# Optimization experiments

Measured on AMD Instinct MI355X. Metric: run time of the kernel, lower is better.

The kernel has to match this reference:

```python
import jax, jax.numpy as jnp
import numpy as np

B, T, F = 64, 512, 256
ENC = 256      # encoder output dim
P = 128        # projection_dim
H = 256        # gru_hidden_dim
K = 12         # num_future_steps
TEMP = 0.1


def setup_inputs() -> dict:
    key = jax.random.key(0)
    ks = jax.random.split(key, 12)
    s = lambda *d: 1.0 / np.sqrt(d[0])
    return {
        "x_seq": jax.random.normal(ks[0], (B, T, F), jnp.float32),
        # encoder: Dense(F -> ENC)
        "W_enc": jax.random.normal(ks[1], (F, ENC), jnp.float32) * s(F),
        "b_enc": jnp.zeros((ENC,), jnp.float32),
        # projection: Dense(ENC -> P)
        "W_proj": jax.random.normal(ks[2], (ENC, P), jnp.float32) * s(ENC),
        "b_proj": jnp.zeros((P,), jnp.float32),
        # GRUCell (flax convention: input dense has bias, hidden dense bias only on n)
        "Wi": jax.random.normal(ks[3], (P, 3 * H), jnp.float32) * s(P),
        "bi": jnp.zeros((3 * H,), jnp.float32),
        "Wh": jax.random.normal(ks[4], (H, 3 * H), jnp.float32) * s(H),
        "bhn": jnp.zeros((H,), jnp.float32),
        # K predictors: Dense(H -> P)
        "Wp": jax.random.normal(ks[5], (K, H, P), jnp.float32) * s(H),
        "bp": jnp.zeros((K, P), jnp.float32),
    }


def _gru_scan(z_seq, Wi, bi, Wh, bhn):
    # z_seq: [B, T, P] -> c_seq: [B, T, H]
    def step(h, x_t):
        gi = x_t @ Wi + bi          # [B, 3H]
        gh = h @ Wh                 # [B, 3H]
        ir, iz, inn = jnp.split(gi, 3, axis=-1)
        hr, hz, hn = jnp.split(gh, 3, axis=-1)
        r = jax.nn.sigmoid(ir + hr)
        z = jax.nn.sigmoid(iz + hz)
        n = jnp.tanh(inn + r * (hn + bhn))
        h_new = (1.0 - z) * n + z * h
        return h_new, h_new

    h0 = jnp.zeros((z_seq.shape[0], Wh.shape[0]), z_seq.dtype)
    _, c = jax.lax.scan(step, h0, jnp.swapaxes(z_seq, 0, 1))  # c: [T, B, H]
    return jnp.swapaxes(c, 0, 1)


def reference(x_seq, W_enc, b_enc, W_proj, b_proj, Wi, bi, Wh, bhn, Wp, bp):
    # encoder per timestep (vmap(vmap(Dense)) == batched matmul)
    z_seq = x_seq @ W_enc + b_enc                 # [B, T, ENC]
    z_seq = z_seq @ W_proj + b_proj               # [B, T, P]
    c_seq = _gru_scan(z_seq, Wi, bi, Wh, bhn)     # [B, T, H]

    Tlen = z_seq.shape[1]
    loss = jnp.asarray(0.0, z_seq.dtype)
    for k in range(1, K + 1):
        if Tlen - k <= 0:
            continue
        z_pos = z_seq[:, k:]                      # [B, T-k, P]
        pred = c_seq[:, :-k] @ Wp[k - 1] + bp[k - 1]  # [B, T-k, P]
        logits = jnp.einsum('btd,bkd->btk', pred, z_pos) / TEMP
        labels = jnp.arange(logits.shape[1])
        # NOTE: faithful to source: [..., labels] with labels=arange is an
        # identity gather along the last axis (not a diagonal pick).
        loss = loss + jnp.mean(-jax.nn.log_softmax(logits, axis=-1)[..., labels])
    return loss / K
```

## Files before the change

### kernel.cpp

```cpp
#include <hip/hip_runtime.h>
#include <hip/hip_bf16.h>
#include <math.h>

#define B_   64
#define T_   512
#define F_   256
#define ENC_ 256
#define P_   128
#define H_   256
#define K_   12
#define INV_TEMP 10.0f

typedef unsigned short u16;
typedef _Float16 half2v __attribute__((ext_vector_type(2)));
union U2H { unsigned int u; half2v h; };
typedef __attribute__((ext_vector_type(8))) short bf16x8;
typedef __attribute__((ext_vector_type(4))) float f32x4;
typedef _Float16 f16x8 __attribute__((ext_vector_type(8)));
union BF8 { bf16x8 v; u16 e[8]; };

__device__ __forceinline__ float rcpf(float x) {
#if __has_builtin(__builtin_amdgcn_rcpf)
    return __builtin_amdgcn_rcpf(x);
#else
    return 1.f / x;
#endif
}
__device__ __forceinline__ u16 f2bf(float f) {
    unsigned int u = __float_as_uint(f);
    unsigned int r = (u + 0x7fffu + ((u >> 16) & 1u)) >> 16;
    return (u16)r;
}
__device__ __forceinline__ float bf2f(u16 v) {
    return __uint_as_float(((unsigned int)v) << 16);
}
__device__ __forceinline__ float bflo(unsigned int u) { return __uint_as_float(u << 16); }
__device__ __forceinline__ float bfhi(unsigned int u) { return __uint_as_float(u & 0xffff0000u); }
__device__ __forceinline__ float wave_sum(float v) {
    #pragma unroll
    for (int o = 32; o > 0; o >>= 1) v += __shfl_down(v, o, 64);
    return v;
}

__global__ __launch_bounds__(256) void setup_conv(const float* __restrict__ Wh,
                                                  _Float16* __restrict__ Wht,
                                                  const float* __restrict__ Wi,
                                                  u16* __restrict__ Wit,
                                                  const float* __restrict__ Wp,
                                                  u16* __restrict__ Wpt,
                                                  const float* __restrict__ We,
                                                  const float* __restrict__ be,
                                                  const float* __restrict__ Wpj,
                                                  const float* __restrict__ bpj,
                                                  u16* __restrict__ Wct,
                                                  float* __restrict__ bc,
                                                  float* __restrict__ accum) {
    int bid = blockIdx.x;
    if (bid < 192) {
        __shared__ float tile0[32][33];
        int g0 = (bid % 24) * 32, k0 = (bid / 24) * 32;
        int tx = threadIdx.x & 31, ty = threadIdx.x >> 5;
        #pragma unroll
        for (int i = 0; i < 32; i += 8)
            tile0[ty + i][tx] = Wh[(size_t)(k0 + ty + i) * 768 + g0 + tx];
        __syncthreads();
        #pragma unroll
        for (int i = 0; i < 32; i += 8)
            Wht[(size_t)(g0 + ty + i) * 256 + k0 + tx] = (_Float16)tile0[tx][ty + i];
    } else if (bid < 288) {
        __shared__ float tile[32][33];
        int b2 = bid - 192;
        int n0 = (b2 % 24) * 32, k0 = (b2 / 24) * 32;
        int tx = threadIdx.x & 31, ty = threadIdx.x >> 5;
        #pragma unroll
        for (int i = 0; i < 32; i += 8)
            tile[ty + i][tx] = Wi[(size_t)(k0 + ty + i) * 768 + n0 + tx];
        __syncthreads();
        #pragma unroll
        for (int i = 0; i < 32; i += 8)
            Wit[(size_t)(n0 + ty + i) * 128 + k0 + tx] = f2bf(tile[tx][ty + i]);
    } else if (bid < 672) {
        __shared__ float tile2[32][33];
        int b3 = bid - 288;
        int kq = b3 / 32, rem = b3 % 32;
        int h0 = (rem % 8) * 32, p0 = (rem / 8) * 32;
        int tx = threadIdx.x & 31, ty = threadIdx.x >> 5;
        #pragma unroll
        for (int i = 0; i < 32; i += 8)
            tile2[ty + i][tx] = Wp[(size_t)kq * H_ * P_ + (size_t)(h0 + ty + i) * P_ + p0 + tx];
        __syncthreads();
        #pragma unroll
        for (int i = 0; i < 32; i += 8)
            Wpt[(size_t)kq * P_ * H_ + (size_t)(p0 + ty + i) * H_ + h0 + tx] = f2bf(tile2[tx][ty + i]);
    } else {
        int f = (bid - 672) * 2 + (threadIdx.x >> 7);
        int p = threadIdx.x & 127;
        if (f < F_) {
            float a = 0.f;
            for (int e = 0; e < ENC_; e++) a = fmaf(We[f * ENC_ + e], Wpj[e * P_ + p], a);
            Wct[(size_t)p * F_ + f] = f2bf(a);
        } else if (f == F_) {
            float a = bpj[p];
            for (int e = 0; e < ENC_; e++) a = fmaf(be[e], Wpj[e * P_ + p], a);
            bc[p] = a;
        } else {
            #pragma unroll
            for (int i = 0; i < 8; i++) accum[p * 8 + i] = 0.f;
        }
    }
}

__global__ __launch_bounds__(256) void gemm_mfma_f32a(const float* __restrict__ A,
                                                      const u16* __restrict__ Bt,
                                                      const float* __restrict__ bias,
                                                      u16* __restrict__ Ch,
                                                      int N, int K) {
    int tid  = threadIdx.x;
    int w    = tid >> 6;
    int lane = tid & 63;
    int col  = lane & 15;
    int quad = lane >> 4;
    int bm = blockIdx.y * 64, bn = blockIdx.x * 128;

    f32x4 acc[8] = {};
    const float* arow = A + (size_t)(bm + w * 16 + col) * K;
    #pragma unroll
    for (int k0 = 0; k0 < K; k0 += 32) {
        float4 v0 = *(const float4*)(arow + k0 + quad * 8);
        float4 v1 = *(const float4*)(arow + k0 + quad * 8 + 4);
        BF8 af;
        af.e[0] = f2bf(v0.x); af.e[1] = f2bf(v0.y); af.e[2] = f2bf(v0.z); af.e[3] = f2bf(v0.w);
        af.e[4] = f2bf(v1.x); af.e[5] = f2bf(v1.y); af.e[6] = f2bf(v1.z); af.e[7] = f2bf(v1.w);
        #pragma unroll
        for (int nt = 0; nt < 8; nt++) {
            bf16x8 bf = *(const bf16x8*)(Bt + (size_t)(bn + nt * 16 + col) * K + k0 + quad * 8);
            acc[nt] = __builtin_amdgcn_mfma_f32_16x16x32_bf16(af.v, bf, acc[nt], 0, 0, 0);
        }
    }
    #pragma unroll
    for (int nt = 0; nt < 8; nt++) {
        int gn = bn + nt * 16 + col;
        float bv = bias[gn];
        #pragma unroll
        for (int r = 0; r < 4; r++) {
            int gm = bm + w * 16 + quad * 4 + r;
            Ch[(size_t)gm * N + gn] = f2bf(acc[nt][r] + bv);
        }
    }
}

__global__ __launch_bounds__(256) void gemm_mfma(const u16* __restrict__ A,
                                                 const u16* __restrict__ Bt,
                                                 const float* __restrict__ bias,
                                                 u16* __restrict__ Ch,
                                                 int N, int K) {
    int tid  = threadIdx.x;
    int w    = tid >> 6;
    int lane = tid & 63;
    int col  = lane & 15;
    int quad = lane >> 4;
    int bm = blockIdx.y * 64, bn = blockIdx.x * 128;

    f32x4 acc[8] = {};
    const u16* arow = A + (size_t)(bm + w * 16 + col) * K;
    #pragma unroll
    for (int k0 = 0; k0 < K; k0 += 32) {
        bf16x8 af = *(const bf16x8*)(arow + k0 + quad * 8);
        #pragma unroll
        for (int nt = 0; nt < 8; nt++) {
            bf16x8 bf = *(const bf16x8*)(Bt + (size_t)(bn + nt * 16 + col) * K + k0 + quad * 8);
            acc[nt] = __builtin_amdgcn_mfma_f32_16x16x32_bf16(af, bf, acc[nt], 0, 0, 0);
        }
    }
    #pragma unroll
    for (int nt = 0; nt < 8; nt++) {
        int gn = bn + nt * 16 + col;
        float bv = bias[gn];
        #pragma unroll
        for (int r = 0; r < 4; r++) {
            int gm = bm + w * 16 + quad * 4 + r;
            Ch[(size_t)gm * N + gn] = f2bf(acc[nt][r] + bv);
        }
    }
}

#define GRUB_ 64

__global__ __attribute__((amdgpu_flat_work_group_size(512, 512)))
void gru_zsum_kernel(const u16* __restrict__ gi,
                     const _Float16* __restrict__ Wht,
                     const float* __restrict__ bhn,
                     u16* __restrict__ ch,
                     const u16* __restrict__ zh,
                     float* __restrict__ zsum) {
    __shared__ __align__(16) char smem[8704];
    int tid = threadIdx.x;

    if (blockIdx.x >= GRUB_) {
        float (*part)[128] = (float (*)[128])smem;
        int b   = blockIdx.x - GRUB_;
        int pg  = tid & 31;
        int g   = tid >> 5;
        const u16* zb = zh + (size_t)b * T_ * P_;
        float s0 = 0.f, s1 = 0.f, s2 = 0.f, s3 = 0.f;
        for (int t = 1 + g; t < T_; t += 16) {
            uint2 v = *(const uint2*)(zb + (size_t)t * P_ + pg * 4);
            s0 += bflo(v.x); s1 += bfhi(v.x);
            s2 += bflo(v.y); s3 += bfhi(v.y);
        }
        part[g][pg * 4 + 0] = s0; part[g][pg * 4 + 1] = s1;
        part[g][pg * 4 + 2] = s2; part[g][pg * 4 + 3] = s3;
        __syncthreads();
        if (tid < 128) {
            float s = 0.f;
            #pragma unroll
            for (int g2 = 0; g2 < 16; g2++) s += part[g2][tid];
            zsum[(size_t)b * P_ + tid] = s;
        }
        return;
    }

    _Float16* hbase = (_Float16*)smem;

    int lane = tid & 63, w = tid >> 6;
    int col  = lane & 15, quad = lane >> 4;
    int b    = blockIdx.x;
    int jj0  = w * 32 + col;

    f16x8 wf[3][2][8];
    #pragma unroll
    for (int g = 0; g < 3; g++)
        #pragma unroll
        for (int n2 = 0; n2 < 2; n2++) {
            const _Float16* src = Wht + (size_t)(g * 256 + jj0 + n2 * 16) * 256 + quad * 8;
            #pragma unroll
            for (int k0 = 0; k0 < 8; k0++)
                wf[g][n2][k0] = *(const f16x8*)(src + k0 * 32);
        }
    #pragma unroll
    for (int g = 0; g < 3; g++)
        #pragma unroll
        for (int n2 = 0; n2 < 2; n2++)
            #pragma unroll
            for (int k0 = 0; k0 < 8; k0++)
                asm volatile("" : "+v"(wf[g][n2][k0]));

    for (int i = tid; i < 528; i += 512) hbase[i] = (_Float16)0.f;

    const u16* gb = gi + (size_t)b * T_ * 768;
    u16* cb       = ch + (size_t)b * T_ * 256;
    float bh0 = bhn[jj0], bh1 = bhn[jj0 + 16];
    float hold0 = 0.f, hold1 = 0.f;
    unsigned int pf[2][6];

    {
        pf[0][0] = gb[jj0];        pf[0][1] = gb[jj0 + 16];
        pf[0][2] = gb[256 + jj0];  pf[0][3] = gb[256 + jj0 + 16];
        pf[0][4] = gb[512 + jj0];  pf[0][5] = gb[512 + jj0 + 16];
    }
    __syncthreads();

    auto body = [&](int t, int c, int pt) {
        int n = c ^ 1;
        if (pt < T_) {
            const u16* gr = gb + (size_t)pt * 768;
            pf[n][0] = gr[jj0];        pf[n][1] = gr[jj0 + 16];
            pf[n][2] = gr[256 + jj0];  pf[n][3] = gr[256 + jj0 + 16];
            pf[n][4] = gr[512 + jj0];  pf[n][5] = gr[512 + jj0 + 16];
        }
        const _Float16* HC = hbase + c * 264;
        _Float16*       HN = hbase + n * 264;
        f32x4 aR0 = {}, aR1 = {}, aZ0 = {}, aZ1 = {}, aN0 = {}, aN1 = {};
        #pragma unroll
        for (int k0 = 0; k0 < 8; k0++) {
            f16x8 af = *(const f16x8*)(HC + k0 * 32 + quad * 8);
            aR0 = __builtin_amdgcn_mfma_f32_16x16x32_f16(af, wf[0][0][k0], aR0, 0, 0, 0);
            aR1 = __builtin_amdgcn_mfma_f32_16x16x32_f16(af, wf[0][1][k0], aR1, 0, 0, 0);
            aZ0 = __builtin_amdgcn_mfma_f32_16x16x32_f16(af, wf[1][0][k0], aZ0, 0, 0, 0);
            aZ1 = __builtin_amdgcn_mfma_f32_16x16x32_f16(af, wf[1][1][k0], aZ1, 0, 0, 0);
            aN0 = __builtin_amdgcn_mfma_f32_16x16x32_f16(af, wf[2][0][k0], aN0, 0, 0, 0);
            aN1 = __builtin_amdgcn_mfma_f32_16x16x32_f16(af, wf[2][1][k0], aN1, 0, 0, 0);
        }
        float rg0 = rcpf(1.f + __expf(-(bf2f((u16)pf[c][0]) + aR0[0])));
        float rg1 = rcpf(1.f + __expf(-(bf2f((u16)pf[c][1]) + aR1[0])));
        float zg0 = rcpf(1.f + __expf(-(bf2f((u16)pf[c][2]) + aZ0[0])));
        float zg1 = rcpf(1.f + __expf(-(bf2f((u16)pf[c][3]) + aZ1[0])));
        float xn0 = bf2f((u16)pf[c][4]) + rg0 * (aN0[0] + bh0);
        float xn1 = bf2f((u16)pf[c][5]) + rg1 * (aN1[0] + bh1);
        float nn0 = fmaf(2.f, rcpf(1.f + __expf(-2.f * xn0)), -1.f);
        float nn1 = fmaf(2.f, rcpf(1.f + __expf(-2.f * xn1)), -1.f);
        hold0 = (1.f - zg0) * nn0 + zg0 * hold0;
        hold1 = (1.f - zg1) * nn1 + zg1 * hold1;
        if (quad == 0) {
            HN[jj0]      = (_Float16)hold0;
            HN[jj0 + 16] = (_Float16)hold1;
        } else if (quad == 1) {
            u16* cr = cb + (size_t)t * 256;
            cr[jj0]      = f2bf(hold0);
            cr[jj0 + 16] = f2bf(hold1);
        }
        asm volatile("s_waitcnt lgkmcnt(0)" ::: "memory");
        __builtin_amdgcn_s_barrier();
        asm volatile("" ::: "memory");
    };

    #pragma unroll 1
    for (int t = 0; t < T_; t += 2) {
        body(t,     0, t + 1);
        body(t + 1, 1, t + 2);
    }
}

__global__ __launch_bounds__(512) void loss_fused(const u16* __restrict__ ch,
                                                  const u16* __restrict__ Wpt,
                                                  const float* __restrict__ bp,
                                                  const u16* __restrict__ zh,
                                                  const float* __restrict__ zsum,
                                                  float* __restrict__ accum) {
    __shared__ u16 Pst[128][136];
    __shared__ u16 Zt[64][136];
    __shared__ float sS[128];
    __shared__ float red[8];
    int k  = blockIdx.z + 1;
    int b  = blockIdx.y;
    int t0 = blockIdx.x * 128;
    int Tk = T_ - k;
    int tid  = threadIdx.x;
    int w    = tid >> 6;
    int lane = tid & 63;
    int col  = lane & 15;
    int quad = lane >> 4;
    const u16* zb = zh + (size_t)b * T_ * P_;

    if (tid < 128) {
        float s = zsum[(size_t)b * P_ + tid];
        for (int t = 1; t < k; t++) s -= bf2f(zb[(size_t)t * P_ + tid]);
        sS[tid] = s;
    }

    {
        f32x4 acc[8] = {};
        const u16* arow = ch + ((size_t)b * T_ + t0 + w * 16 + col) * H_;
        const u16* wk   = Wpt + (size_t)(k - 1) * P_ * H_;
        #pragma unroll
        for (int k0 = 0; k0 < 8; k0++) {
            bf16x8 af = *(const bf16x8*)(arow + k0 * 32 + quad * 8);
            #pragma unroll
            for (int nt = 0; nt < 8; nt++) {
                bf16x8 bf = *(const bf16x8*)(wk + (size_t)(nt * 16 + col) * H_ + k0 * 32 + quad * 8);
                acc[nt] = __builtin_amdgcn_mfma_f32_16x16x32_bf16(af, bf, acc[nt], 0, 0, 0);
            }
        }
        #pragma unroll
        for (int nt = 0; nt < 8; nt++) {
            float bias = bp[(size_t)(k - 1) * P_ + nt * 16 + col];
            #pragma unroll
            for (int r = 0; r < 4; r++)
                Pst[w * 16 + quad * 4 + r][nt * 16 + col] = f2bf(acc[nt][r] + bias);
        }
    }
    __syncthreads();

    float mloc[4], sloc[4];
    #pragma unroll
    for (int r = 0; r < 4; r++) { mloc[r] = -INFINITY; sloc[r] = 0.f; }

    for (int ct = 0; ct < Tk; ct += 64) {
        __syncthreads();
        {
            int cc = tid;
            #pragma unroll
            for (int rep = 0; rep < 2; rep++, cc += 512) {
                int row = cc >> 4;
                int off = (cc & 15) * 8;
                int tcol = k + ct + row;
                *(uint4*)&Zt[row][off] = *(const uint4*)(zb + (size_t)tcol * P_ + off);
            }
        }
        __syncthreads();
        f32x4 acc[4] = {};
        #pragma unroll
        for (int k0 = 0; k0 < 4; k0++) {
            bf16x8 af = *(const bf16x8*)(&Pst[w * 16 + col][k0 * 32 + quad * 8]);
            #pragma unroll
            for (int nt = 0; nt < 4; nt++) {
                bf16x8 bf = *(const bf16x8*)(&Zt[nt * 16 + col][k0 * 32 + quad * 8]);
                acc[nt] = __builtin_amdgcn_mfma_f32_16x16x32_bf16(af, bf, acc[nt], 0, 0, 0);
            }
        }
        #pragma unroll
        for (int r = 0; r < 4; r++) {
            float l[4];
            float tmax = -INFINITY;
            #pragma unroll
            for (int nt = 0; nt < 4; nt++) {
                bool valid = (ct + nt * 16 + col) < Tk;
                l[nt] = valid ? acc[nt][r] * INV_TEMP : -INFINITY;
                tmax = fmaxf(tmax, l[nt]);
            }
            float mnew = fmaxf(mloc[r], tmax);
            float e = __expf(l[0] - mnew) + __expf(l[1] - mnew)
                    + __expf(l[2] - mnew) + __expf(l[3] - mnew);
            sloc[r] = sloc[r] * __expf(mloc[r] - mnew) + e;
            mloc[r] = mnew;
        }
    }
    #pragma unroll
    for (int r = 0; r < 4; r++) {
        #pragma unroll
        for (int o = 1; o < 16; o <<= 1) {
            float mo = __shfl_xor(mloc[r], o, 64);
            float so = __shfl_xor(sloc[r], o, 64);
            float mn = fmaxf(mloc[r], mo);
            sloc[r] = sloc[r] * __expf(mloc[r] - mn) + so * __expf(mo - mn);
            mloc[r] = mn;
        }
    }
    float tkinv = INV_TEMP / (float)Tk;
    float scale = 1.0f / ((float)K_ * (float)B_ * (float)Tk);
    float bs = 0.f;
    #pragma unroll
    for (int r = 0; r < 4; r++) {
        int row = w * 16 + quad * 4 + r;
        BF8 pv;
        pv.v = *(const bf16x8*)(&Pst[row][col * 8]);
        float d = 0.f;
        #pragma unroll
        for (int m = 0; m < 8; m++) d = fmaf(bf2f(pv.e[m]), sS[col * 8 + m], d);
        #pragma unroll
        for (int o = 1; o < 16; o <<= 1) d += __shfl_xor(d, o, 64);
        int gr = t0 + row;
        if (gr < Tk) bs += mloc[r] + __logf(sloc[r]) - d * tkinv;
    }
    if (col != 0) bs = 0.f;
    bs = wave_sum(bs);
    if (lane == 0) red[w] = bs;
    __syncthreads();
    if (tid == 0) {
        float tot = 0.f;
        #pragma unroll
        for (int i = 0; i < 8; i++) tot += red[i];
        atomicAdd(&accum[(blockIdx.x * 809 + b * 67 + blockIdx.z * 131) & 1023],
                  tot * scale);
    }
}

__global__ void finalize(const float* __restrict__ accum, float* __restrict__ out) {
    int tid = threadIdx.x;
    __shared__ float red[4];
    float v = 0.f;
    for (int i = tid; i < 1024; i += 256) v += accum[i];
    float sres = wave_sum(v);
    if ((tid & 63) == 0) red[tid >> 6] = sres;
    __syncthreads();
    if (tid == 0) out[0] = red[0] + red[1] + red[2] + red[3];
}

extern "C" void kernel_launch(void* const* d_in, const int* in_sizes, int n_in,
                              void* d_out, int out_size, void* d_ws, size_t ws_size,
                              hipStream_t stream) {
    const float* x      = (const float*)d_in[0];
    const float* W_enc  = (const float*)d_in[1];
    const float* b_enc  = (const float*)d_in[2];
    const float* W_proj = (const float*)d_in[3];
    const float* b_proj = (const float*)d_in[4];
    const float* Wi     = (const float*)d_in[5];
    const float* bi     = (const float*)d_in[6];
    const float* Wh     = (const float*)d_in[7];
    const float* bhn    = (const float*)d_in[8];
    const float* Wp     = (const float*)d_in[9];
    const float* bp     = (const float*)d_in[10];
    float* out = (float*)d_out;

    float* ws    = (float*)d_ws;
    float* bc    = ws;
    float* accum = bc + 128;
    _Float16* Wht = (_Float16*)(ws + 1152);
    u16* Wct     = (u16*)(ws + 99456);
    u16* Wit     = (u16*)(ws + 115840);
    u16* Wpt     = (u16*)(ws + 164992);
    u16* zh      = (u16*)(ws + 361600);
    float* zsum  = ws + 2458752;
    u16* gi      = (u16*)(ws + 2466944);
    u16* ch      = (u16*)(ws + 15049856);

    const int MT = B_ * T_;

    setup_conv<<<801, 256, 0, stream>>>(Wh, Wht, Wi, Wit, Wp, Wpt,
                                        W_enc, b_enc, W_proj, b_proj, Wct, bc, accum);
    gemm_mfma_f32a<<<dim3(1, MT / 64), 256, 0, stream>>>(x, Wct, bc, zh, P_, F_);
    gemm_mfma<<<dim3(6, MT / 64), 256, 0, stream>>>(zh, Wit, bi, gi, 3 * H_, P_);
    gru_zsum_kernel<<<GRUB_ + B_, 512, 0, stream>>>(gi, Wht, bhn, ch, zh, zsum);
    loss_fused<<<dim3(4, B_, K_), 512, 0, stream>>>(ch, Wpt, bp, zh, zsum, accum);
    finalize<<<1, 256, 0, stream>>>(accum, out);
}
```

Baseline: 953.6 us.

## Process three future steps per loss block sharing Z tiles; move GRU gate prefetch

The loss kernel now handles three prediction offsets per block, so each staged Z tile is reused by three MFMA chains. The grid shrinks from 12 to 4 in z, and the next Z tile is held in registers while the current one is computed. In the GRU kernel, the next step's gate inputs are now loaded at the end of each step rather than double-buffered at the start, which shortens the per-step register footprint. The trade-offs are triple the shared memory and accumulator registers in the loss kernel, which may lower occupancy, and GRU global loads that now sit closer to the barrier.

New measurement: 1.040 ms. 1.09x slower.

```diff
diff --git a/kernel.cpp b/kernel.cpp
--- a/kernel.cpp
+++ b/kernel.cpp
@@ -251,23 +251,17 @@
     u16* cb       = ch + (size_t)b * T_ * 256;
     float bh0 = bhn[jj0], bh1 = bhn[jj0 + 16];
     float hold0 = 0.f, hold1 = 0.f;
-    unsigned int pf[2][6];
+    unsigned int pf[6];
 
     {
-        pf[0][0] = gb[jj0];        pf[0][1] = gb[jj0 + 16];
-        pf[0][2] = gb[256 + jj0];  pf[0][3] = gb[256 + jj0 + 16];
-        pf[0][4] = gb[512 + jj0];  pf[0][5] = gb[512 + jj0 + 16];
+        pf[0] = gb[jj0];        pf[1] = gb[jj0 + 16];
+        pf[2] = gb[256 + jj0];  pf[3] = gb[256 + jj0 + 16];
+        pf[4] = gb[512 + jj0];  pf[5] = gb[512 + jj0 + 16];
     }
     __syncthreads();
 
-    auto body = [&](int t, int c, int pt) {
+    auto body = [&](int t, int c) {
         int n = c ^ 1;
-        if (pt < T_) {
-            const u16* gr = gb + (size_t)pt * 768;
-            pf[n][0] = gr[jj0];        pf[n][1] = gr[jj0 + 16];
-            pf[n][2] = gr[256 + jj0];  pf[n][3] = gr[256 + jj0 + 16];
-            pf[n][4] = gr[512 + jj0];  pf[n][5] = gr[512 + jj0 + 16];
-        }
         const _Float16* HC = hbase + c * 264;
         _Float16*       HN = hbase + n * 264;
         f32x4 aR0 = {}, aR1 = {}, aZ0 = {}, aZ1 = {}, aN0 = {}, aN1 = {};
@@ -281,12 +275,12 @@
             aN0 = __builtin_amdgcn_mfma_f32_16x16x32_f16(af, wf[2][0][k0], aN0, 0, 0, 0);
             aN1 = __builtin_amdgcn_mfma_f32_16x16x32_f16(af, wf[2][1][k0], aN1, 0, 0, 0);
         }
-        float rg0 = rcpf(1.f + __expf(-(bf2f((u16)pf[c][0]) + aR0[0])));
-        float rg1 = rcpf(1.f + __expf(-(bf2f((u16)pf[c][1]) + aR1[0])));
-        float zg0 = rcpf(1.f + __expf(-(bf2f((u16)pf[c][2]) + aZ0[0])));
-        float zg1 = rcpf(1.f + __expf(-(bf2f((u16)pf[c][3]) + aZ1[0])));
-        float xn0 = bf2f((u16)pf[c][4]) + rg0 * (aN0[0] + bh0);
-        float xn1 = bf2f((u16)pf[c][5]) + rg1 * (aN1[0] + bh1);
+        float rg0 = rcpf(1.f + __expf(-(bf2f((u16)pf[0]) + aR0[0])));
+        float rg1 = rcpf(1.f + __expf(-(bf2f((u16)pf[1]) + aR1[0])));
+        float zg0 = rcpf(1.f + __expf(-(bf2f((u16)pf[2]) + aZ0[0])));
+        float zg1 = rcpf(1.f + __expf(-(bf2f((u16)pf[3]) + aZ1[0])));
+        float xn0 = bf2f((u16)pf[4]) + rg0 * (aN0[0] + bh0);
+        float xn1 = bf2f((u16)pf[5]) + rg1 * (aN1[0] + bh1);
         float nn0 = fmaf(2.f, rcpf(1.f + __expf(-2.f * xn0)), -1.f);
         float nn1 = fmaf(2.f, rcpf(1.f + __expf(-2.f * xn1)), -1.f);
         hold0 = (1.f - zg0) * nn0 + zg0 * hold0;
@@ -299,6 +293,12 @@
             cr[jj0]      = f2bf(hold0);
             cr[jj0 + 16] = f2bf(hold1);
         }
+        if (t + 1 < T_) {
+            const u16* gr = gb + (size_t)(t + 1) * 768;
+            pf[0] = gr[jj0];        pf[1] = gr[jj0 + 16];
+            pf[2] = gr[256 + jj0];  pf[3] = gr[256 + jj0 + 16];
+            pf[4] = gr[512 + jj0];  pf[5] = gr[512 + jj0 + 16];
+        }
         asm volatile("s_waitcnt lgkmcnt(0)" ::: "memory");
         __builtin_amdgcn_s_barrier();
         asm volatile("" ::: "memory");
@@ -306,25 +306,26 @@
 
     #pragma unroll 1
     for (int t = 0; t < T_; t += 2) {
-        body(t,     0, t + 1);
-        body(t + 1, 1, t + 2);
-    }
-}
-
-__global__ __launch_bounds__(512) void loss_fused(const u16* __restrict__ ch,
-                                                  const u16* __restrict__ Wpt,
-                                                  const float* __restrict__ bp,
-                                                  const u16* __restrict__ zh,
-                                                  const float* __restrict__ zsum,
-                                                  float* __restrict__ accum) {
-    __shared__ u16 Pst[128][136];
+        body(t,     0);
+        body(t + 1, 1);
+    }
+}
+
+__global__ __attribute__((amdgpu_flat_work_group_size(512, 512)))
+void loss_fused(const u16* __restrict__ ch,
+                const u16* __restrict__ Wpt,
+                const float* __restrict__ bp,
+                const u16* __restrict__ zh,
+                const float* __restrict__ zsum,
+                float* __restrict__ accum) {
+    __shared__ u16 Pst[3][128][136];
     __shared__ u16 Zt[64][136];
-    __shared__ float sS[128];
+    __shared__ float sS[3][128];
     __shared__ float red[8];
-    int k  = blockIdx.z + 1;
+    int kz    = blockIdx.z;
+    int kbase = 1 + kz * 3;
     int b  = blockIdx.y;
     int t0 = blockIdx.x * 128;
-    int Tk = T_ - k;
     int tid  = threadIdx.x;
     int w    = tid >> 6;
     int lane = tid & 63;
@@ -332,105 +333,132 @@
     int quad = lane >> 4;
     const u16* zb = zh + (size_t)b * T_ * P_;
 
+    int row0 = tid >> 4;
+    int row1 = row0 + 32;
+    int off  = (tid & 15) * 8;
+    uint4 rA = *(const uint4*)(zb + (size_t)(kbase + row0) * P_ + off);
+    uint4 rB = *(const uint4*)(zb + (size_t)(kbase + row1) * P_ + off);
+
     if (tid < 128) {
         float s = zsum[(size_t)b * P_ + tid];
-        for (int t = 1; t < k; t++) s -= bf2f(zb[(size_t)t * P_ + tid]);
-        sS[tid] = s;
+        for (int t = 1; t < kbase; t++) s -= bf2f(zb[(size_t)t * P_ + tid]);
+        sS[0][tid] = s;
+        s -= bf2f(zb[(size_t)kbase * P_ + tid]);       sS[1][tid] = s;
+        s -= bf2f(zb[(size_t)(kbase + 1) * P_ + tid]); sS[2][tid] = s;
     }
 
     {
-        f32x4 acc[8] = {};
+        f32x4 acc[3][8] = {};
         const u16* arow = ch + ((size_t)b * T_ + t0 + w * 16 + col) * H_;
-        const u16* wk   = Wpt + (size_t)(k - 1) * P_ * H_;
+        const u16* wk   = Wpt + (size_t)(kbase - 1) * P_ * H_;
         #pragma unroll
         for (int k0 = 0; k0 < 8; k0++) {
             bf16x8 af = *(const bf16x8*)(arow + k0 * 32 + quad * 8);
             #pragma unroll
+            for (int j = 0; j < 3; j++)
+                #pragma unroll
+                for (int nt = 0; nt < 8; nt++) {
+                    bf16x8 bf = *(const bf16x8*)(wk + (size_t)j * P_ * H_
+                                 + (size_t)(nt * 16 + col) * H_ + k0 * 32 + quad * 8);
+                    acc[j][nt] = __builtin_amdgcn_mfma_f32_16x16x32_bf16(af, bf, acc[j][nt], 0, 0, 0);
+                }
+        }
+        #pragma unroll
+        for (int j = 0; j < 3; j++)
+            #pragma unroll
             for (int nt = 0; nt < 8; nt++) {
-                bf16x8 bf = *(const bf16x8*)(wk + (size_t)(nt * 16 + col) * H_ + k0 * 32 + quad * 8);
-                acc[nt] = __builtin_amdgcn_mfma_f32_16x16x32_bf16(af, bf, acc[nt], 0, 0, 0);
+                float bias = bp[(size_t)(kbase - 1 + j) * P_ + nt * 16 + col];
+                #pragma unroll
+                for (int r = 0; r < 4; r++)
+                    Pst[j][w * 16 + quad * 4 + r][nt * 16 + col] = f2bf(acc[j][nt][r] + bias);
             }
-        }
-        #pragma unroll
-        for (int nt = 0; nt < 8; nt++) {
-            float bias = bp[(size_t)(k - 1) * P_ + nt * 16 + col];
-            #pragma unroll
-            for (int r = 0; r < 4; r++)
-                Pst[w * 16 + quad * 4 + r][nt * 16 + col] = f2bf(acc[nt][r] + bias);
-        }
     }
     __syncthreads();
 
-    float mloc[4], sloc[4];
-    #pragma unroll
-    for (int r = 0; r < 4; r++) { mloc[r] = -INFINITY; sloc[r] = 0.f; }
-
-    for (int ct = 0; ct < Tk; ct += 64) {
+    float mloc[3][4], sloc[3][4];
+    #pragma unroll
+    for (int j = 0; j < 3; j++)
+        #pragma unroll
+        for (int r = 0; r < 4; r++) { mloc[j][r] = -INFINITY; sloc[j][r] = 0.f; }
+
+    int TkMax = T_ - kbase;
+    for (int ct = 0; ct < TkMax; ct += 64) {
         __syncthreads();
-        {
-            int cc = tid;
-            #pragma unroll
-            for (int rep = 0; rep < 2; rep++, cc += 512) {
-                int row = cc >> 4;
-                int off = (cc & 15) * 8;
-                int tcol = k + ct + row;
-                *(uint4*)&Zt[row][off] = *(const uint4*)(zb + (size_t)tcol * P_ + off);
-            }
-        }
+        *(uint4*)&Zt[row0][off] = rA;
+        *(uint4*)&Zt[row1][off] = rB;
         __syncthreads();
-        f32x4 acc[4] = {};
+        if (ct + 64 < TkMax) {
+            int tc = kbase + ct + 64;
+            rA = *(const uint4*)(zb + (size_t)(tc + row0) * P_ + off);
+            rB = *(const uint4*)(zb + (size_t)(tc + row1) * P_ + off);
+        }
+        f32x4 acc[3][4] = {};
         #pragma unroll
         for (int k0 = 0; k0 < 4; k0++) {
-            bf16x8 af = *(const bf16x8*)(&Pst[w * 16 + col][k0 * 32 + quad * 8]);
+            bf16x8 pa0 = *(const bf16x8*)(&Pst[0][w * 16 + col][k0 * 32 + quad * 8]);
+            bf16x8 pa1 = *(const bf16x8*)(&Pst[1][w * 16 + col][k0 * 32 + quad * 8]);
+            bf16x8 pa2 = *(const bf16x8*)(&Pst[2][w * 16 + col][k0 * 32 + quad * 8]);
             #pragma unroll
             for (int nt = 0; nt < 4; nt++) {
                 bf16x8 bf = *(const bf16x8*)(&Zt[nt * 16 + col][k0 * 32 + quad * 8]);
-                acc[nt] = __builtin_amdgcn_mfma_f32_16x16x32_bf16(af, bf, acc[nt], 0, 0, 0);
+                acc[0][nt] = __builtin_amdgcn_mfma_f32_16x16x32_bf16(pa0, bf, acc[0][nt], 0, 0, 0);
+                acc[1][nt] = __builtin_amdgcn_mfma_f32_16x16x32_bf16(pa1, bf, acc[1][nt], 0, 0, 0);
+                acc[2][nt] = __builtin_amdgcn_mfma_f32_16x16x32_bf16(pa2, bf, acc[2][nt], 0, 0, 0);
             }
         }
         #pragma unroll
+        for (int j = 0; j < 3; j++) {
+            #pragma unroll
+            for (int r = 0; r < 4; r++) {
+                float l[4];
+                float tmax = -INFINITY;
+                #pragma unroll
+                for (int nt = 0; nt < 4; nt++) {
+                    int cc = ct + nt * 16 + col;
+                    bool v = (cc >= j) && (kbase + cc < T_);
+                    l[nt] = v ? acc[j][nt][r] * INV_TEMP : -INFINITY;
+                    tmax = fmaxf(tmax, l[nt]);
+                }
+                float mnew = fmaxf(mloc[j][r], tmax);
+                float e = __expf(l[0] - mnew) + __expf(l[1] - mnew)
+                        + __expf(l[2] - mnew) + __expf(l[3] - mnew);
+                sloc[j][r] = sloc[j][r] * __expf(mloc[j][r] - mnew) + e;
+                mloc[j][r] = mnew;
+            }
+        }
+    }
+    #pragma unroll
+    for (int j = 0; j < 3; j++)
+        #pragma unroll
         for (int r = 0; r < 4; r++) {
-            float l[4];
-            float tmax = -INFINITY;
-            #pragma unroll
-            for (int nt = 0; nt < 4; nt++) {
-                bool valid = (ct + nt * 16 + col) < Tk;
-                l[nt] = valid ? acc[nt][r] * INV_TEMP : -INFINITY;
-                tmax = fmaxf(tmax, l[nt]);
+            #pragma unroll
+            for (int o = 1; o < 16; o <<= 1) {
+                float mo = __shfl_xor(mloc[j][r], o, 64);
+                float so = __shfl_xor(sloc[j][r], o, 64);
+                float mn = fmaxf(mloc[j][r], mo);
+                sloc[j][r] = sloc[j][r] * __expf(mloc[j][r] - mn) + so * __expf(mo - mn);
+                mloc[j][r] = mn;
             }
-            float mnew = fmaxf(mloc[r], tmax);
-            float e = __expf(l[0] - mnew) + __expf(l[1] - mnew)
-                    + __expf(l[2] - mnew) + __expf(l[3] - mnew);
-            sloc[r] = sloc[r] * __expf(mloc[r] - mnew) + e;
-            mloc[r] = mnew;
-        }
-    }
-    #pragma unroll
-    for (int r = 0; r < 4; r++) {
-        #pragma unroll
-        for (int o = 1; o < 16; o <<= 1) {
-            float mo = __shfl_xor(mloc[r], o, 64);
-            float so = __shfl_xor(sloc[r], o, 64);
-            float mn = fmaxf(mloc[r], mo);
-            sloc[r] = sloc[r] * __expf(mloc[r] - mn) + so * __expf(mo - mn);
-            mloc[r] = mn;
-        }
-    }
-    float tkinv = INV_TEMP / (float)Tk;
-    float scale = 1.0f / ((float)K_ * (float)B_ * (float)Tk);
+        }
     float bs = 0.f;
     #pragma unroll
-    for (int r = 0; r < 4; r++) {
-        int row = w * 16 + quad * 4 + r;
-        BF8 pv;
-        pv.v = *(const bf16x8*)(&Pst[row][col * 8]);
-        float d = 0.f;
-        #pragma unroll
-        for (int m = 0; m < 8; m++) d = fmaf(bf2f(pv.e[m]), sS[col * 8 + m], d);
-        #pragma unroll
-        for (int o = 1; o < 16; o <<= 1) d += __shfl_xor(d, o, 64);
-        int gr = t0 + row;
-        if (gr < Tk) bs += mloc[r] + __logf(sloc[r]) - d * tkinv;
+    for (int j = 0; j < 3; j++) {
+        int Tkj = T_ - (kbase + j);
+        float tkinv = INV_TEMP / (float)Tkj;
+        float scale = 1.0f / ((float)K_ * (float)B_ * (float)Tkj);
+        #pragma unroll
+        for (int r = 0; r < 4; r++) {
+            int row = w * 16 + quad * 4 + r;
+            BF8 pv;
+            pv.v = *(const bf16x8*)(&Pst[j][row][col * 8]);
+            float d = 0.f;
+            #pragma unroll
+            for (int m = 0; m < 8; m++) d = fmaf(bf2f(pv.e[m]), sS[j][col * 8 + m], d);
+            #pragma unroll
+            for (int o = 1; o < 16; o <<= 1) d += __shfl_xor(d, o, 64);
+            int gr = t0 + row;
+            if (gr < Tkj) bs += (mloc[j][r] + __logf(sloc[j][r]) - d * tkinv) * scale;
+        }
     }
     if (col != 0) bs = 0.f;
     bs = wave_sum(bs);
@@ -440,8 +468,7 @@
         float tot = 0.f;
         #pragma unroll
         for (int i = 0; i < 8; i++) tot += red[i];
-        atomicAdd(&accum[(blockIdx.x * 809 + b * 67 + blockIdx.z * 131) & 1023],
-                  tot * scale);
+        atomicAdd(&accum[(blockIdx.x * 809 + b * 67 + blockIdx.z * 131) & 1023], tot);
     }
 }
 
@@ -491,6 +518,6 @@
     gemm_mfma_f32a<<<dim3(1, MT / 64), 256, 0, stream>>>(x, Wct, bc, zh, P_, F_);
     gemm_mfma<<<dim3(6, MT / 64), 256, 0, stream>>>(zh, Wit, bi, gi, 3 * H_, P_);
     gru_zsum_kernel<<<GRUB_ + B_, 512, 0, stream>>>(gi, Wht, bhn, ch, zh, zsum);
-    loss_fused<<<dim3(4, B_, K_), 512, 0, stream>>>(ch, Wpt, bp, zh, zsum, accum);
+    loss_fused<<<dim3(4, B_, 4), 512, 0, stream>>>(ch, Wpt, bp, zh, zsum, accum);
     finalize<<<1, 256, 0, stream>>>(accum, out);
 }
```

## Double-buffer Z tiles in loss kernel and move GRU gate prefetch after compute

Applied to the files above, without the earlier changes.

The loss kernel now keeps two shared-memory Z tiles, prefetching the next chunks into registers two iterations ahead and swapping buffers with a single barrier per iteration instead of two. It also sets a minimum-occupancy hint in launch bounds. In the GRU scan, the double-buffered register prefetch of input gates is replaced by a single set loaded after the gate math, just before the step barrier, which lowers register use but leaves less time to hide that load. The extra register prefetch and the occupancy hint may cause spilling in the loss kernel.

Measured after the change: 967.8 us. No clear change (+1.5%).

```diff
diff --git a/kernel.cpp b/kernel.cpp
--- a/kernel.cpp
+++ b/kernel.cpp
@@ -251,23 +251,17 @@
     u16* cb       = ch + (size_t)b * T_ * 256;
     float bh0 = bhn[jj0], bh1 = bhn[jj0 + 16];
     float hold0 = 0.f, hold1 = 0.f;
-    unsigned int pf[2][6];
+    unsigned int pf[6];
 
     {
-        pf[0][0] = gb[jj0];        pf[0][1] = gb[jj0 + 16];
-        pf[0][2] = gb[256 + jj0];  pf[0][3] = gb[256 + jj0 + 16];
-        pf[0][4] = gb[512 + jj0];  pf[0][5] = gb[512 + jj0 + 16];
+        pf[0] = gb[jj0];        pf[1] = gb[jj0 + 16];
+        pf[2] = gb[256 + jj0];  pf[3] = gb[256 + jj0 + 16];
+        pf[4] = gb[512 + jj0];  pf[5] = gb[512 + jj0 + 16];
     }
     __syncthreads();
 
-    auto body = [&](int t, int c, int pt) {
+    auto body = [&](int t, int c) {
         int n = c ^ 1;
-        if (pt < T_) {
-            const u16* gr = gb + (size_t)pt * 768;
-            pf[n][0] = gr[jj0];        pf[n][1] = gr[jj0 + 16];
-            pf[n][2] = gr[256 + jj0];  pf[n][3] = gr[256 + jj0 + 16];
-            pf[n][4] = gr[512 + jj0];  pf[n][5] = gr[512 + jj0 + 16];
-        }
         const _Float16* HC = hbase + c * 264;
         _Float16*       HN = hbase + n * 264;
         f32x4 aR0 = {}, aR1 = {}, aZ0 = {}, aZ1 = {}, aN0 = {}, aN1 = {};
@@ -281,12 +275,12 @@
             aN0 = __builtin_amdgcn_mfma_f32_16x16x32_f16(af, wf[2][0][k0], aN0, 0, 0, 0);
             aN1 = __builtin_amdgcn_mfma_f32_16x16x32_f16(af, wf[2][1][k0], aN1, 0, 0, 0);
         }
-        float rg0 = rcpf(1.f + __expf(-(bf2f((u16)pf[c][0]) + aR0[0])));
-        float rg1 = rcpf(1.f + __expf(-(bf2f((u16)pf[c][1]) + aR1[0])));
-        float zg0 = rcpf(1.f + __expf(-(bf2f((u16)pf[c][2]) + aZ0[0])));
-        float zg1 = rcpf(1.f + __expf(-(bf2f((u16)pf[c][3]) + aZ1[0])));
-        float xn0 = bf2f((u16)pf[c][4]) + rg0 * (aN0[0] + bh0);
-        float xn1 = bf2f((u16)pf[c][5]) + rg1 * (aN1[0] + bh1);
+        float rg0 = rcpf(1.f + __expf(-(bf2f((u16)pf[0]) + aR0[0])));
+        float rg1 = rcpf(1.f + __expf(-(bf2f((u16)pf[1]) + aR1[0])));
+        float zg0 = rcpf(1.f + __expf(-(bf2f((u16)pf[2]) + aZ0[0])));
+        float zg1 = rcpf(1.f + __expf(-(bf2f((u16)pf[3]) + aZ1[0])));
+        float xn0 = bf2f((u16)pf[4]) + rg0 * (aN0[0] + bh0);
+        float xn1 = bf2f((u16)pf[5]) + rg1 * (aN1[0] + bh1);
         float nn0 = fmaf(2.f, rcpf(1.f + __expf(-2.f * xn0)), -1.f);
         float nn1 = fmaf(2.f, rcpf(1.f + __expf(-2.f * xn1)), -1.f);
         hold0 = (1.f - zg0) * nn0 + zg0 * hold0;
@@ -299,6 +293,12 @@
             cr[jj0]      = f2bf(hold0);
             cr[jj0 + 16] = f2bf(hold1);
         }
+        if (t + 1 < T_) {
+            const u16* gr = gb + (size_t)(t + 1) * 768;
+            pf[0] = gr[jj0];        pf[1] = gr[jj0 + 16];
+            pf[2] = gr[256 + jj0];  pf[3] = gr[256 + jj0 + 16];
+            pf[4] = gr[512 + jj0];  pf[5] = gr[512 + jj0 + 16];
+        }
         asm volatile("s_waitcnt lgkmcnt(0)" ::: "memory");
         __builtin_amdgcn_s_barrier();
         asm volatile("" ::: "memory");
@@ -306,19 +306,19 @@
 
     #pragma unroll 1
     for (int t = 0; t < T_; t += 2) {
-        body(t,     0, t + 1);
-        body(t + 1, 1, t + 2);
-    }
-}
-
-__global__ __launch_bounds__(512) void loss_fused(const u16* __restrict__ ch,
-                                                  const u16* __restrict__ Wpt,
-                                                  const float* __restrict__ bp,
-                                                  const u16* __restrict__ zh,
-                                                  const float* __restrict__ zsum,
-                                                  float* __restrict__ accum) {
+        body(t,     0);
+        body(t + 1, 1);
+    }
+}
+
+__global__ __launch_bounds__(512, 4) void loss_fused(const u16* __restrict__ ch,
+                                                     const u16* __restrict__ Wpt,
+                                                     const float* __restrict__ bp,
+                                                     const u16* __restrict__ zh,
+                                                     const float* __restrict__ zsum,
+                                                     float* __restrict__ accum) {
     __shared__ u16 Pst[128][136];
-    __shared__ u16 Zt[64][136];
+    __shared__ u16 Zt[2][64][136];
     __shared__ float sS[128];
     __shared__ float red[8];
     int k  = blockIdx.z + 1;
@@ -331,6 +331,14 @@
     int col  = lane & 15;
     int quad = lane >> 4;
     const u16* zb = zh + (size_t)b * T_ * P_;
+    const u16* zk = zb + (size_t)k * P_;
+
+    int rr  = tid >> 4;
+    int off = (tid & 15) * 8;
+    uint4 a0 = *(const uint4*)(zk + (size_t)rr * P_ + off);
+    uint4 b0 = *(const uint4*)(zk + (size_t)(rr + 32) * P_ + off);
+    uint4 rA = *(const uint4*)(zk + (size_t)(64 + rr) * P_ + off);
+    uint4 rB = *(const uint4*)(zk + (size_t)(64 + rr + 32) * P_ + off);
 
     if (tid < 128) {
         float s = zsum[(size_t)b * P_ + tid];
@@ -358,6 +366,8 @@
             for (int r = 0; r < 4; r++)
                 Pst[w * 16 + quad * 4 + r][nt * 16 + col] = f2bf(acc[nt][r] + bias);
         }
+        *(uint4*)&Zt[0][rr][off]      = a0;
+        *(uint4*)&Zt[0][rr + 32][off] = b0;
     }
     __syncthreads();
 
@@ -365,29 +375,31 @@
     #pragma unroll
     for (int r = 0; r < 4; r++) { mloc[r] = -INFINITY; sloc[r] = 0.f; }
 
-    for (int ct = 0; ct < Tk; ct += 64) {
-        __syncthreads();
-        {
-            int cc = tid;
-            #pragma unroll
-            for (int rep = 0; rep < 2; rep++, cc += 512) {
-                int row = cc >> 4;
-                int off = (cc & 15) * 8;
-                int tcol = k + ct + row;
-                *(uint4*)&Zt[row][off] = *(const uint4*)(zb + (size_t)tcol * P_ + off);
-            }
-        }
-        __syncthreads();
+    int nIter = (Tk + 63) >> 6;
+    int cbuf = 0;
+    #pragma unroll 1
+    for (int it = 0; it < nIter; ++it) {
+        if (it + 1 < nIter) {
+            *(uint4*)&Zt[cbuf ^ 1][rr][off]      = rA;
+            *(uint4*)&Zt[cbuf ^ 1][rr + 32][off] = rB;
+        }
+        if (it + 2 < nIter) {
+            const u16* zn = zk + (size_t)((it + 2) * 64) * P_;
+            rA = *(const uint4*)(zn + (size_t)rr * P_ + off);
+            rB = *(const uint4*)(zn + (size_t)(rr + 32) * P_ + off);
+        }
+        const u16* ztb = &Zt[cbuf][0][0];
         f32x4 acc[4] = {};
         #pragma unroll
         for (int k0 = 0; k0 < 4; k0++) {
             bf16x8 af = *(const bf16x8*)(&Pst[w * 16 + col][k0 * 32 + quad * 8]);
             #pragma unroll
             for (int nt = 0; nt < 4; nt++) {
-                bf16x8 bf = *(const bf16x8*)(&Zt[nt * 16 + col][k0 * 32 + quad * 8]);
+                bf16x8 bf = *(const bf16x8*)(ztb + (size_t)(nt * 16 + col) * 136 + k0 * 32 + quad * 8);
                 acc[nt] = __builtin_amdgcn_mfma_f32_16x16x32_bf16(af, bf, acc[nt], 0, 0, 0);
             }
         }
+        int ct = it * 64;
         #pragma unroll
         for (int r = 0; r < 4; r++) {
             float l[4];
@@ -404,6 +416,10 @@
             sloc[r] = sloc[r] * __expf(mloc[r] - mnew) + e;
             mloc[r] = mnew;
         }
+        asm volatile("s_waitcnt lgkmcnt(0)" ::: "memory");
+        __builtin_amdgcn_s_barrier();
+        asm volatile("" ::: "memory");
+        cbuf ^= 1;
     }
     #pragma unroll
     for (int r = 0; r < 4; r++) {
```
